# Kernel tuning notes

Measured on AMD Instinct MI355X. Metric: run time of the kernel, lower is better.

Reference implementation:

```python
import jax, jax.numpy as jnp
import numpy as np

DIM = 1024
HDIM = 128
SEQ = 2048
B = 4
NHEADS = DIM // HDIM


def _decay_mask(seq_len, gamma):
    idx = jnp.arange(seq_len, dtype=jnp.float32)
    # gamma ** (i - j), lower-triangular (i >= j), else 0
    D = gamma ** (idx[:, None] - idx[None, :])
    D = jnp.where(idx[:, None] >= idx[None, :], D, 0.0)
    return D.astype(jnp.float32)


def setup_inputs() -> dict:
    key = jax.random.key(0)
    ks = jax.random.split(key, 8)
    q = jax.random.normal(ks[0], (B, SEQ, DIM), dtype=jnp.float32)
    k = jax.random.normal(ks[1], (B, SEQ, DIM), dtype=jnp.float32)
    v = jax.random.normal(ks[2], (B, SEQ, DIM), dtype=jnp.float32)
    # per-head shared QKV weight (source reuses one Dense for Q,K,V)
    scale = 1.0 / np.sqrt(HDIM)
    W_qkv = jax.random.normal(ks[3], (NHEADS, HDIM, HDIM), dtype=jnp.float32) * scale
    # gate: Dense(dim, bias, swish); output: Dense(dim, bias)
    Wg = jax.random.normal(ks[4], (DIM, DIM), dtype=jnp.float32) / np.sqrt(DIM)
    bg = jnp.zeros((DIM,), dtype=jnp.float32)
    Wo = jax.random.normal(ks[5], (DIM, DIM), dtype=jnp.float32) / np.sqrt(DIM)
    bo = jnp.zeros((DIM,), dtype=jnp.float32)
    # GroupNormalization(scale=False): default groups=32, center=True -> beta only
    beta = jnp.zeros((DIM,), dtype=jnp.float32)
    return {"q": q, "k": k, "v": v, "W_qkv": W_qkv, "Wg": Wg, "bg": bg,
            "Wo": Wo, "bo": bo, "beta": beta}


def _retention_head(qh, kh, vh, W, D):
    # qh,kh,vh: [B,S,HDIM]; source bug: all three come from q, and the
    # single shared Dense W projects each.
    Q = qh @ W
    K = kh @ W
    V = vh @ W
    x = jnp.einsum('bsd,btd->bst', Q, K) / jnp.sqrt(jnp.float32(HDIM))
    # D normalized: D / sqrt(sum over axis 1 (rows), broadcast over rows)
    Dn = D / jnp.sqrt(jnp.sum(D, axis=0))  # tf.reduce_sum(D,1) on [S,S]: axis=1 of 2D = cols? see note
    x = x * Dn
    # row-norm: divide by max(|sum over axis 1 of each [S,S] slice|, 1)
    s = jnp.sum(x, axis=1, keepdims=True)  # per-sample, tf axis 1 of [S,S]
    x = x / jnp.maximum(jnp.abs(s), 1.0)
    return jnp.einsum('bst,btd->bsd', x, V)


def _group_norm(x, beta, groups=32, eps=1e-3):
    b, s, c = x.shape
    xg = x.reshape(b, s, groups, c // groups)
    mu = jnp.mean(xg, axis=-1, keepdims=True)
    var = jnp.var(xg, axis=-1, keepdims=True)
    xn = (xg - mu) / jnp.sqrt(var + eps)
    return xn.reshape(b, s, c) + beta


def reference(q, k, v, W_qkv, Wg, bg, Wo, bo, beta):
    gammas = 1.0 - 2.0 ** (-5.0 - jnp.arange(NHEADS, dtype=jnp.float32))
    Wgate = jax.nn.swish(q @ Wg + bg)
    # source bug: splits q for Q, K, V alike
    qs = q.reshape(B, SEQ, NHEADS, HDIM)
    outs = []
    idx = jnp.arange(SEQ, dtype=jnp.float32)
    lower = idx[:, None] >= idx[None, :]
    for h in range(NHEADS):
        D = jnp.where(lower, gammas[h] ** (idx[:, None] - idx[None, :]), 0.0)
        qh = qs[:, :, h, :]
        outs.append(_retention_head(qh, qh, qh, W_qkv[h], D))
    x = jnp.concatenate(outs, axis=-1)
    Y = _group_norm(x, beta)
    return (Wgate * Y) @ Wo + bo
```

## Files before the change

kernel.cpp:

```cpp
#include <hip/hip_runtime.h>


constexpr int SEQ  = 2048;
constexpr int BATCH= 4;
constexpr int DIM  = 1024;
constexpr int HDIM = 128;
constexpr int NH   = 8;
constexpr int NBH  = BATCH * NH;
constexpr int NC   = 16;
constexpr int CCH  = 32;
constexpr int NCC  = SEQ / CCH;

typedef __bf16 bf16x8 __attribute__((ext_vector_type(8)));
typedef float  f32x4  __attribute__((ext_vector_type(4)));

__device__ __forceinline__ f32x4 mfma16(bf16x8 a, bf16x8 b, f32x4 c) {
  return __builtin_amdgcn_mfma_f32_16x16x32_bf16(a, b, c, 0, 0, 0);
}

__device__ __forceinline__ float bf2f(unsigned short u) {
  return __builtin_bit_cast(float, (unsigned int)u << 16);
}
__device__ __forceinline__ unsigned short f2bf(float f) {
  unsigned int x = __builtin_bit_cast(unsigned int, f);
  x += 0x7fffu + ((x >> 16) & 1u);
  return (unsigned short)(x >> 16);
}

__device__ __forceinline__ int swz(int row, int col, int RS) {
  int cb  = col >> 3;
  int scb = (cb & ~7) | ((cb ^ (row >> 1)) & 7);
  return row * RS + scb * 8 + (col & 7);
}

__device__ __forceinline__ uint4 pack8(float4 a, float4 b) {
  uint4 o;
  o.x = (unsigned int)f2bf(a.x) | ((unsigned int)f2bf(a.y) << 16);
  o.y = (unsigned int)f2bf(a.z) | ((unsigned int)f2bf(a.w) << 16);
  o.z = (unsigned int)f2bf(b.x) | ((unsigned int)f2bf(b.y) << 16);
  o.w = (unsigned int)f2bf(b.z) | ((unsigned int)f2bf(b.w) << 16);
  return o;
}

__global__ void detect(const unsigned short* __restrict__ q, int* __restrict__ flag)
{
  int lane = threadIdx.x;
  int sane = 0;
  for (int i = lane; i < 1024; i += 64) {
    int e = (q[i] >> 7) & 0xFF;
    sane += (e >= 100 && e <= 140) ? 1 : 0;
  }
  #pragma unroll
  for (int o = 1; o < 64; o <<= 1) sane += __shfl_xor(sane, o);
  if (lane == 0) flag[0] = (sane >= 900) ? 1 : 0;
}

__global__ __launch_bounds__(256) void wtrans(const void* __restrict__ src,
    unsigned short* __restrict__ dst, int rows, int cols,
    const int* __restrict__ dflag)
{
  __shared__ float tile[64][65];
  const int isbf = dflag[0];
  const size_t moff = (size_t)blockIdx.z * rows * cols;
  const int r0 = blockIdx.y * 64, c0 = blockIdx.x * 64;
  const int tr = threadIdx.x >> 4;
  const int tc = (threadIdx.x & 15) * 4;

  #pragma unroll
  for (int rr = 0; rr < 64; rr += 16) {
    int r = r0 + rr + tr;
    if (isbf) {
      const unsigned short* s = (const unsigned short*)src + moff + (size_t)r * cols + c0 + tc;
      tile[rr + tr][tc + 0] = bf2f(s[0]);
      tile[rr + tr][tc + 1] = bf2f(s[1]);
      tile[rr + tr][tc + 2] = bf2f(s[2]);
      tile[rr + tr][tc + 3] = bf2f(s[3]);
    } else {
      float4 v = *(const float4*)((const float*)src + moff + (size_t)r * cols + c0 + tc);
      tile[rr + tr][tc + 0] = v.x;
      tile[rr + tr][tc + 1] = v.y;
      tile[rr + tr][tc + 2] = v.z;
      tile[rr + tr][tc + 3] = v.w;
    }
  }
  __syncthreads();

  const int n  = threadIdx.x >> 2;
  const int kg = (threadIdx.x & 3) * 16;
  unsigned int ov[8];
  #pragma unroll
  for (int j = 0; j < 8; ++j) {
    unsigned short lo = f2bf(tile[kg + 2 * j + 0][n]);
    unsigned short hi = f2bf(tile[kg + 2 * j + 1][n]);
    ov[j] = (unsigned int)lo | ((unsigned int)hi << 16);
  }
  unsigned short* d = dst + moff + (size_t)(c0 + n) * rows + r0 + kg;
  ((uint4*)d)[0] = make_uint4(ov[0], ov[1], ov[2], ov[3]);
  ((uint4*)d)[1] = make_uint4(ov[4], ov[5], ov[6], ov[7]);
}

__global__ __launch_bounds__(256, 4) void gemm128(
    const void* __restrict__ A, int lda,
    const unsigned short* __restrict__ B, int ldb, int K,
    const void* __restrict__ bias, int act,
    void* __restrict__ out, int mode, int adt, int obf,
    const int* __restrict__ dflag)
{
  __shared__ __align__(16) unsigned short As[128 * 64];
  __shared__ __align__(16) unsigned short Bs[128 * 64];
  const int isbf = dflag[0];
  const int abf  = (adt == 1) || (adt == 2 && isbf);
  const int tid  = threadIdx.x;
  const int lane = tid & 63;
  const int w    = tid >> 6;
  const int wy   = w >> 1, wx = w & 1;
  const int m15  = lane & 15, qd = lane >> 4;

  int bx = blockIdx.x, by = blockIdx.y;
  if (mode == 0) {
    int nwg = gridDim.x * gridDim.y;
    int lin = by * gridDim.x + bx;
    int qq = nwg >> 3, rr = nwg & 7;
    int xcd = lin & 7, idx = lin >> 3;
    int wg = (xcd < rr) ? xcd * (qq + 1) + idx
                        : rr * (qq + 1) + (xcd - rr) * qq + idx;
    bx = wg % gridDim.x;
    by = wg / gridDim.x;
  }

  const size_t aoff = (mode == 1) ? (size_t)blockIdx.z * 128 : 0;
  const size_t boff = (mode == 1) ? (size_t)blockIdx.z * 128 * 128 : 0;
  const size_t arow = (size_t)(by * 128);
  const size_t bcol = (size_t)(bx * 128);

  f32x4 zero4 = {0.0f, 0.0f, 0.0f, 0.0f};
  f32x4 acc[4][4];
  #pragma unroll
  for (int i = 0; i < 4; ++i)
    #pragma unroll
    for (int j = 0; j < 4; ++j) acc[i][j] = zero4;

  const int kIters = K >> 6;
  for (int kt = 0; kt < kIters; ++kt) {
    __syncthreads();
    if (abf) {
      const unsigned short* pa = (const unsigned short*)A + aoff + arow * lda + kt * 64;
      #pragma unroll
      for (int g = 0; g < 4; ++g) {
        int idx = tid + g * 256;
        int r = idx >> 3, cb = idx & 7;
        *(uint4*)&As[swz(r, cb * 8, 64)] = *(const uint4*)(pa + (size_t)r * lda + cb * 8);
      }
    } else {
      const float* pa = (const float*)A + aoff + arow * lda + kt * 64;
      #pragma unroll
      for (int g = 0; g < 4; ++g) {
        int idx = tid + g * 256;
        int r = idx >> 3, cb = idx & 7;
        float4 f0 = *(const float4*)(pa + (size_t)r * lda + cb * 8);
        float4 f1 = *(const float4*)(pa + (size_t)r * lda + cb * 8 + 4);
        *(uint4*)&As[swz(r, cb * 8, 64)] = pack8(f0, f1);
      }
    }
    {
      const unsigned short* pb = B + boff + bcol * (size_t)ldb + kt * 64;
      #pragma unroll
      for (int g = 0; g < 4; ++g) {
        int idx = tid + g * 256;
        int r = idx >> 3, cb = idx & 7;
        *(uint4*)&Bs[swz(r, cb * 8, 64)] = *(const uint4*)(pb + (size_t)r * ldb + cb * 8);
      }
    }
    __syncthreads();
    #pragma unroll
    for (int kk = 0; kk < 2; ++kk) {
      bf16x8 af[4], bfr[4];
      #pragma unroll
      for (int mt = 0; mt < 4; ++mt)
        af[mt] = *(const bf16x8*)&As[swz(wy * 64 + mt * 16 + m15, kk * 32 + qd * 8, 64)];
      #pragma unroll
      for (int nt = 0; nt < 4; ++nt)
        bfr[nt] = *(const bf16x8*)&Bs[swz(wx * 64 + nt * 16 + m15, kk * 32 + qd * 8, 64)];
      #pragma unroll
      for (int mt = 0; mt < 4; ++mt)
        #pragma unroll
        for (int nt = 0; nt < 4; ++nt)
          acc[mt][nt] = mfma16(af[mt], bfr[nt], acc[mt][nt]);
    }
  }

  const int obf_eff = (obf == 2) ? (isbf ? 1 : 0) : obf;
  #pragma unroll
  for (int mt = 0; mt < 4; ++mt)
    #pragma unroll
    for (int nt = 0; nt < 4; ++nt) {
      int nl = wx * 64 + nt * 16 + m15;
      int n  = bx * 128 + nl;
      float bv = 0.0f;
      if (bias) bv = isbf ? bf2f(((const unsigned short*)bias)[n]) : ((const float*)bias)[n];
      #pragma unroll
      for (int r = 0; r < 4; ++r) {
        int ml = wy * 64 + mt * 16 + qd * 4 + r;
        int m  = by * 128 + ml;
        float v = acc[mt][nt][r] + bv;
        if (act == 1) v = v / (1.0f + __expf(-v));
        if (mode == 0) {
          size_t oi = (size_t)m * (gridDim.x * 128) + n;
          if (obf_eff) ((unsigned short*)out)[oi] = f2bf(v);
          else         ((float*)out)[oi] = v;
        } else {
          int b = m >> 11, s = m & 2047;
          size_t bh = (size_t)(b * NH + blockIdx.z);
          ((unsigned short*)out)[(bh * SEQ + s) * HDIM + n] = f2bf(v);
        }
      }
    }
}

__global__ __launch_bounds__(128) void kzcA(const unsigned short* __restrict__ X,
                                            float* __restrict__ L)
{
  const int d  = threadIdx.x;
  const int cc = blockIdx.x;
  const int bh = blockIdx.y;
  const int h  = bh & 7;
  const float gam = 1.0f - exp2f(-5.0f - (float)h);
  const unsigned short* Xb = X + (size_t)bh * SEQ * HDIM + (size_t)cc * CCH * HDIM;
  float z = 0.0f;
  #pragma unroll
  for (int i = CCH - 1; i >= 0; --i)
    z = bf2f(Xb[(size_t)i * HDIM + d]) + gam * z;
  L[((size_t)bh * NCC + cc) * HDIM + d] = z;
}

__global__ __launch_bounds__(128) void kzcB(float* __restrict__ L)
{
  const int d  = threadIdx.x;
  const int bh = blockIdx.x;
  const int h  = bh & 7;
  const float gam = 1.0f - exp2f(-5.0f - (float)h);
  const float g32 = exp2f(log2f(gam) * (float)CCH);
  float z = 0.0f;
  for (int cc = NCC - 1; cc >= 0; --cc) {
    size_t i = ((size_t)bh * NCC + cc) * HDIM + d;
    float lc = L[i];
    L[i] = z;
    z = lc + g32 * z;
  }
}

__global__ __launch_bounds__(64) void kdot2(const unsigned short* __restrict__ X,
    const float* __restrict__ Carry, float* __restrict__ U)
{
  const int lane = threadIdx.x;
  const int cc   = blockIdx.x;
  const int bh   = blockIdx.y;
  const int h    = bh & 7;
  const float gam    = 1.0f - exp2f(-5.0f - (float)h);
  const float l2g    = log2f(gam);
  const float inv1mg = exp2f(5.0f + (float)h);
  const float c1     = 0.08838834764831845f;
  const unsigned short* Xb = X + (size_t)bh * SEQ * HDIM + (size_t)cc * CCH * HDIM;
  float2 cr = *(const float2*)(Carry + ((size_t)bh * NCC + cc) * HDIM + lane * 2);
  float z0 = 0.0f, z1 = 0.0f;
  float coeff = gam;
  float keep = 0.0f;
  #pragma unroll
  for (int i = 0; i < CCH; ++i) {
    const int t = CCH - 1 - i;
    unsigned int xu = *(const unsigned int*)(Xb + (size_t)t * HDIM + lane * 2);
    float x0 = bf2f((unsigned short)(xu & 0xffffu));
    float x1 = bf2f((unsigned short)(xu >> 16));
    z0 = x0 + gam * z0;
    z1 = x1 + gam * z1;
    float dot = x0 * (z0 + coeff * cr.x) + x1 * (z1 + coeff * cr.y);
    #pragma unroll
    for (int o = 1; o < 64; o <<= 1) dot += __shfl_xor(dot, o);
    if (lane == t) keep = dot;
    coeff *= gam;
  }
  if (lane < CCH) {
    int tg = cc * CCH + lane;
    float colD   = (1.0f - exp2f(l2g * (float)(SEQ - tg))) * inv1mg;
    float sq     = sqrtf(colD);
    float colsum = keep * c1 / sq;
    float den    = fmaxf(fabsf(colsum), 1.0f);
    U[(size_t)bh * SEQ + tg] = c1 / (sq * den);
  }
}

__global__ __launch_bounds__(256, 2) void chunkstate(
    const unsigned short* __restrict__ X,
    const float* __restrict__ U,
    unsigned short* __restrict__ G)
{
  __shared__ __align__(16) unsigned short XT [16384];
  __shared__ __align__(16) unsigned short XTs[16384];
  const int tid  = threadIdx.x;
  const int lane = tid & 63;
  const int w    = tid >> 6;
  const int wy   = w >> 1, wx = w & 1;
  const int m15  = lane & 15, qd = lane >> 4;
  const int c    = blockIdx.x;
  const int bh   = blockIdx.y;
  const int h    = bh & 7;
  const float gam = 1.0f - exp2f(-5.0f - (float)h);
  const float l2g = log2f(gam);
  const int t0 = c * 128;
  const unsigned short* Xb = X + (size_t)bh * SEQ * HDIM;
  const float* Ub = U + (size_t)bh * SEQ;

  #pragma unroll
  for (int g = 0; g < 8; ++g) {
    int idx = tid + g * 256;
    int t = idx >> 4, d0 = (idx & 15) * 8;
    uint4 w4 = *(const uint4*)(Xb + (size_t)(t0 + t) * HDIM + d0);
    float wt = exp2f(l2g * (float)(127 - t)) * Ub[t0 + t];
    const unsigned short* wp = (const unsigned short*)&w4;
    #pragma unroll
    for (int j = 0; j < 8; ++j) {
      unsigned short v = wp[j];
      XT [swz(d0 + j, t, 128)] = v;
      XTs[swz(d0 + j, t, 128)] = f2bf(bf2f(v) * wt);
    }
  }
  __syncthreads();

  f32x4 zero4 = {0.0f, 0.0f, 0.0f, 0.0f};
  f32x4 acc[4][4];
  #pragma unroll
  for (int i = 0; i < 4; ++i)
    #pragma unroll
    for (int j = 0; j < 4; ++j) acc[i][j] = zero4;

  #pragma unroll
  for (int kk = 0; kk < 4; ++kk) {
    bf16x8 af[4], bfr[4];
    #pragma unroll
    for (int mt = 0; mt < 4; ++mt)
      af[mt] = *(const bf16x8*)&XTs[swz(wy * 64 + mt * 16 + m15, kk * 32 + qd * 8, 128)];
    #pragma unroll
    for (int nt = 0; nt < 4; ++nt)
      bfr[nt] = *(const bf16x8*)&XT[swz(wx * 64 + nt * 16 + m15, kk * 32 + qd * 8, 128)];
    #pragma unroll
    for (int mt = 0; mt < 4; ++mt)
      #pragma unroll
      for (int nt = 0; nt < 4; ++nt)
        acc[mt][nt] = mfma16(af[mt], bfr[nt], acc[mt][nt]);
  }

  unsigned short* Gp = G + (((size_t)bh * NC + c) << 14);
  #pragma unroll
  for (int mt = 0; mt < 4; ++mt)
    #pragma unroll
    for (int nt = 0; nt < 4; ++nt)
      #pragma unroll
      for (int r = 0; r < 4; ++r) {
        int d1 = wy * 64 + mt * 16 + qd * 4 + r;
        int d2 = wx * 64 + nt * 16 + m15;
        Gp[(size_t)d1 * 128 + d2] = f2bf(acc[mt][nt][r]);
      }
}

__global__ __launch_bounds__(256) void scanS(unsigned short* __restrict__ GS)
{
  int gid = blockIdx.x * 256 + threadIdx.x;
  int bh = gid >> 11;
  int e8 = (gid & 2047) << 3;
  int h  = bh & 7;
  float gam  = 1.0f - exp2f(-5.0f - (float)h);
  float g128 = exp2f(log2f(gam) * 128.0f);
  float s[8];
  #pragma unroll
  for (int j = 0; j < 8; ++j) s[j] = 0.0f;
  unsigned short* base = GS + ((size_t)bh << 18) + e8;
  #pragma unroll
  for (int c = 0; c < NC; ++c) {
    uint4 v = *(uint4*)(base + ((size_t)c << 14));
    const unsigned short* wp = (const unsigned short*)&v;
    #pragma unroll
    for (int j = 0; j < 8; ++j) s[j] = g128 * s[j] + bf2f(wp[j]);
    uint4 o;
    unsigned int* op = (unsigned int*)&o;
    op[0] = (unsigned int)f2bf(s[0]) | ((unsigned int)f2bf(s[1]) << 16);
    op[1] = (unsigned int)f2bf(s[2]) | ((unsigned int)f2bf(s[3]) << 16);
    op[2] = (unsigned int)f2bf(s[4]) | ((unsigned int)f2bf(s[5]) << 16);
    op[3] = (unsigned int)f2bf(s[6]) | ((unsigned int)f2bf(s[7]) << 16);
    *(uint4*)(base + ((size_t)c << 14)) = o;
  }
}

__global__ __launch_bounds__(256, 2) void retention2(
    const unsigned short* __restrict__ X,
    const float* __restrict__ U,
    const unsigned short* __restrict__ S,
    unsigned short* __restrict__ R)
{
  __shared__ __align__(16) unsigned short Qs[16384];
  __shared__ __align__(16) unsigned short SB[16384];

  const int tid  = threadIdx.x;
  const int lane = tid & 63;
  const int w    = tid >> 6;
  const int wy   = w >> 1, wx = w & 1;
  const int m15  = lane & 15, qd = lane >> 4;
  const int c    = blockIdx.x;
  const int bh   = blockIdx.y;
  const int h    = bh & 7;
  const int b    = bh >> 3;
  const float gam = 1.0f - exp2f(-5.0f - (float)h);
  const float l2g = log2f(gam);
  const int sbase = c * 128;
  const unsigned short* Xb = X + (size_t)bh * SEQ * HDIM;
  const float* Ub = U + (size_t)bh * SEQ;

  #pragma unroll
  for (int g = 0; g < 8; ++g) {
    int idx = tid + g * 256;
    int r = idx >> 4, cb = idx & 15;
    *(uint4*)&Qs[swz(r, cb * 8, 128)] =
        *(const uint4*)(Xb + (size_t)(sbase + r) * HDIM + cb * 8);
  }
  if (c > 0) {
    const unsigned short* Sp = S + (((size_t)bh * NC + (c - 1)) << 14);
    #pragma unroll
    for (int g = 0; g < 8; ++g) {
      int idx = tid + g * 256;
      int r = idx >> 4, cb = idx & 15;
      *(uint4*)&SB[swz(r, cb * 8, 128)] = *(const uint4*)(Sp + (size_t)r * 128 + cb * 8);
    }
  }
  __syncthreads();

  bf16x8 aq[4][4];
  #pragma unroll
  for (int mt = 0; mt < 4; ++mt)
    #pragma unroll
    for (int kk = 0; kk < 4; ++kk)
      aq[mt][kk] = *(const bf16x8*)&Qs[swz(wy * 64 + mt * 16 + m15, kk * 32 + qd * 8, 128)];

  float crowL[16];
  #pragma unroll
  for (int mt = 0; mt < 4; ++mt)
    #pragma unroll
    for (int r = 0; r < 4; ++r)
      crowL[mt * 4 + r] = exp2f(l2g * (float)(wy * 64 + mt * 16 + qd * 4 + r));

  f32x4 zero4 = {0.0f, 0.0f, 0.0f, 0.0f};
  f32x4 oacc[4][4];
  #pragma unroll
  for (int i = 0; i < 4; ++i)
    #pragma unroll
    for (int j = 0; j < 4; ++j) oacc[i][j] = zero4;

  if (c > 0) {
    #pragma unroll
    for (int kk = 0; kk < 4; ++kk) {
      bf16x8 bs[4];
      #pragma unroll
      for (int nt = 0; nt < 4; ++nt)
        bs[nt] = *(const bf16x8*)&SB[swz(wx * 64 + nt * 16 + m15, kk * 32 + qd * 8, 128)];
      #pragma unroll
      for (int mt = 0; mt < 4; ++mt)
        #pragma unroll
        for (int nt = 0; nt < 4; ++nt)
          oacc[mt][nt] = mfma16(aq[mt][kk], bs[nt], oacc[mt][nt]);
    }
    #pragma unroll
    for (int mt = 0; mt < 4; ++mt) {
      #pragma unroll
      for (int r = 0; r < 4; ++r) {
        float f = crowL[mt * 4 + r] * gam;
        #pragma unroll
        for (int nt = 0; nt < 4; ++nt) oacc[mt][nt][r] *= f;
      }
    }
  }

  unsigned short* VsT = SB;
  unsigned short* Ps  = SB + 8192;

  for (int th = 0; th < 2; ++th) {
    const int t0 = th * 64;
    f32x4 pacc[4][2];
    #pragma unroll
    for (int i = 0; i < 4; ++i) { pacc[i][0] = zero4; pacc[i][1] = zero4; }
    #pragma unroll
    for (int kk = 0; kk < 4; ++kk) {
      bf16x8 bk[2];
      #pragma unroll
      for (int nt = 0; nt < 2; ++nt)
        bk[nt] = *(const bf16x8*)&Qs[swz(t0 + wx * 32 + nt * 16 + m15, kk * 32 + qd * 8, 128)];
      #pragma unroll
      for (int mt = 0; mt < 4; ++mt)
        #pragma unroll
        for (int nt = 0; nt < 2; ++nt)
          pacc[mt][nt] = mfma16(aq[mt][kk], bk[nt], pacc[mt][nt]);
    }
    __syncthreads();

    #pragma unroll
    for (int g = 0; g < 4; ++g) {
      int idx = tid + g * 256;
      int t = idx & 63, d0 = (idx >> 6) * 8;
      uint4 w4 = *(const uint4*)(Xb + (size_t)(sbase + t0 + t) * HDIM + d0);
      const unsigned short* wp = (const unsigned short*)&w4;
      #pragma unroll
      for (int j = 0; j < 8; ++j)
        VsT[swz(d0 + j, t, 64)] = wp[j];
    }
    #pragma unroll
    for (int nt = 0; nt < 2; ++nt) {
      int tloc = t0 + wx * 32 + nt * 16 + m15;
      float cf = exp2f(-l2g * (float)tloc) * Ub[sbase + tloc];
      #pragma unroll
      for (int mt = 0; mt < 4; ++mt)
        #pragma unroll
        for (int r = 0; r < 4; ++r) {
          int sl = wy * 64 + mt * 16 + qd * 4 + r;
          float v = (sl >= tloc) ? pacc[mt][nt][r] * crowL[mt * 4 + r] * cf : 0.0f;
          Ps[swz(sl, tloc - t0, 64)] = f2bf(v);
        }
    }
    __syncthreads();
    #pragma unroll
    for (int kk = 0; kk < 2; ++kk) {
      bf16x8 ap[4], bv[4];
      #pragma unroll
      for (int mt = 0; mt < 4; ++mt)
        ap[mt] = *(const bf16x8*)&Ps[swz(wy * 64 + mt * 16 + m15, kk * 32 + qd * 8, 64)];
      #pragma unroll
      for (int nt = 0; nt < 4; ++nt)
        bv[nt] = *(const bf16x8*)&VsT[swz(wx * 64 + nt * 16 + m15, kk * 32 + qd * 8, 64)];
      #pragma unroll
      for (int mt = 0; mt < 4; ++mt)
        #pragma unroll
        for (int nt = 0; nt < 4; ++nt)
          oacc[mt][nt] = mfma16(ap[mt], bv[nt], oacc[mt][nt]);
    }
  }

  #pragma unroll
  for (int mt = 0; mt < 4; ++mt)
    #pragma unroll
    for (int nt = 0; nt < 4; ++nt)
      #pragma unroll
      for (int r = 0; r < 4; ++r) {
        int sg = sbase + wy * 64 + mt * 16 + qd * 4 + r;
        int n  = wx * 64 + nt * 16 + m15;
        R[(size_t)(b * SEQ + sg) * DIM + h * HDIM + n] = f2bf(oacc[mt][nt][r]);
      }
}

__global__ __launch_bounds__(256) void gn_gate(const unsigned short* __restrict__ R,
    const void* __restrict__ beta, unsigned short* __restrict__ GU,
    const int* __restrict__ dflag)
{
  const int isbf = dflag[0];
  const int row = blockIdx.x;
  const int t   = threadIdx.x;
  uint2 xv = *(const uint2*)(R + (size_t)row * DIM + t * 4);
  float x0 = bf2f((unsigned short)(xv.x & 0xffffu)), x1 = bf2f((unsigned short)(xv.x >> 16));
  float x2 = bf2f((unsigned short)(xv.y & 0xffffu)), x3 = bf2f((unsigned short)(xv.y >> 16));
  float s  = x0 + x1 + x2 + x3;
  float ss = x0 * x0 + x1 * x1 + x2 * x2 + x3 * x3;
  #pragma unroll
  for (int m = 1; m <= 4; m <<= 1) {
    s  += __shfl_xor(s, m, 8);
    ss += __shfl_xor(ss, m, 8);
  }
  float mean = s * (1.0f / 32.0f);
  float var  = ss * (1.0f / 32.0f) - mean * mean;
  float rstd = rsqrtf(var + 1e-3f);
  float b0, b1, b2, b3;
  if (isbf) {
    uint2 bv = *(const uint2*)((const unsigned short*)beta + t * 4);
    b0 = bf2f((unsigned short)(bv.x & 0xffffu)); b1 = bf2f((unsigned short)(bv.x >> 16));
    b2 = bf2f((unsigned short)(bv.y & 0xffffu)); b3 = bf2f((unsigned short)(bv.y >> 16));
  } else {
    float4 bv = *(const float4*)((const float*)beta + t * 4);
    b0 = bv.x; b1 = bv.y; b2 = bv.z; b3 = bv.w;
  }
  uint2 gv = *(const uint2*)(GU + (size_t)row * DIM + t * 4);
  float g0 = bf2f((unsigned short)(gv.x & 0xffffu)), g1 = bf2f((unsigned short)(gv.x >> 16));
  float g2 = bf2f((unsigned short)(gv.y & 0xffffu)), g3 = bf2f((unsigned short)(gv.y >> 16));
  unsigned short u0 = f2bf(((x0 - mean) * rstd + b0) * g0);
  unsigned short u1 = f2bf(((x1 - mean) * rstd + b1) * g1);
  unsigned short u2 = f2bf(((x2 - mean) * rstd + b2) * g2);
  unsigned short u3 = f2bf(((x3 - mean) * rstd + b3) * g3);
  uint2 o;
  o.x = (unsigned int)u0 | ((unsigned int)u1 << 16);
  o.y = (unsigned int)u2 | ((unsigned int)u3 << 16);
  *(uint2*)(GU + (size_t)row * DIM + t * 4) = o;
}

extern "C" void kernel_launch(void* const* d_in, const int* in_sizes, int n_in,
                              void* d_out, int out_size, void* d_ws, size_t ws_size,
                              hipStream_t stream)
{
  (void)in_sizes; (void)n_in; (void)out_size; (void)ws_size;
  const void* q    = d_in[0];
  const void* Wqkv = d_in[3];
  const void* Wg   = d_in[4];
  const void* bg   = d_in[5];
  const void* Wo   = d_in[6];
  const void* bo   = d_in[7];
  const void* beta = d_in[8];

  char* p = (char*)d_ws;
  auto take = [&](size_t bytes) { char* r = p; p += (bytes + 255) & ~(size_t)255; return r; };
  int*  flag = (int*)take(256);
  unsigned short* X  = (unsigned short*)take((size_t)NBH * SEQ * HDIM * 2);
  float* U     = (float*)take((size_t)NBH * SEQ * 4);
  unsigned short* WqkvT = (unsigned short*)take((size_t)NH * HDIM * HDIM * 2);
  unsigned short* WgT   = (unsigned short*)take((size_t)DIM * DIM * 2);
  unsigned short* WoT   = (unsigned short*)take((size_t)DIM * DIM * 2);
  unsigned short* Rb = (unsigned short*)d_out;
  unsigned short* GS = (unsigned short*)((char*)d_out + (size_t)16 * 1024 * 1024);
  float* Carry = (float*)GS;
  unsigned short* Gg = X;

  detect<<<1, 64, 0, stream>>>((const unsigned short*)q, flag);

  wtrans<<<dim3(16, 16, 1), 256, 0, stream>>>(Wg,   WgT,   DIM,  DIM,  flag);
  wtrans<<<dim3(16, 16, 1), 256, 0, stream>>>(Wo,   WoT,   DIM,  DIM,  flag);
  wtrans<<<dim3(2, 2, NH),  256, 0, stream>>>(Wqkv, WqkvT, HDIM, HDIM, flag);

  gemm128<<<dim3(1, 64, NH), 256, 0, stream>>>(q, DIM, WqkvT, HDIM, HDIM,
                                               nullptr, 0, X, 1, 2, 1, flag);

  kzcA <<<dim3(NCC, NBH), 128, 0, stream>>>(X, Carry);
  kzcB <<<NBH, 128, 0, stream>>>(Carry);
  kdot2<<<dim3(NCC, NBH), 64, 0, stream>>>(X, Carry, U);

  chunkstate<<<dim3(NC, NBH), 256, 0, stream>>>(X, U, GS);
  scanS     <<<256, 256, 0, stream>>>(GS);
  retention2<<<dim3(NC, NBH), 256, 0, stream>>>(X, U, GS, Rb);

  gemm128<<<dim3(8, 64, 1), 256, 0, stream>>>(q, DIM, WgT, DIM, DIM, bg, 1,
                                              Gg, 0, 2, 1, flag);

  gn_gate<<<dim3(BATCH * SEQ, 1, 1), 256, 0, stream>>>(Rb, beta, Gg, flag);

  gemm128<<<dim3(8, 64, 1), 256, 0, stream>>>(Gg, DIM, WoT, DIM, DIM, bo, 0,
                                              d_out, 0, 1, 2, flag);
}
```

Before: 345.8 us.

## Pre-convert q to bf16, use direct global-to-LDS loads, coalesce epilogue stores

Adds a kernel that converts q to bf16 once into workspace so both the QKV and gate GEMMs take the bf16 path. The GEMM tile loads use global_load_lds to write directly into swizzled LDS instead of going through registers. The epilogues of the head-projection GEMM, chunkstate and retention2 stage results through LDS so global stores are 16-byte coalesced rather than scattered 2-byte writes. The cost is an extra conversion pass over q plus more workspace and extra barriers in the epilogues.

```diff
diff --git a/kernel.cpp b/kernel.cpp
--- a/kernel.cpp
+++ b/kernel.cpp
@@ -33,6 +33,12 @@
   return row * RS + scb * 8 + (col & 7);
 }
 
+typedef const __attribute__((address_space(1))) unsigned int* gas_t;
+typedef __attribute__((address_space(3))) unsigned int* las_t;
+__device__ __forceinline__ void gl_lds16(const unsigned short* g, unsigned short* l) {
+  __builtin_amdgcn_global_load_lds((gas_t)g, (las_t)l, 16, 0, 0);
+}
+
 __device__ __forceinline__ uint4 pack8(float4 a, float4 b) {
   uint4 o;
   o.x = (unsigned int)f2bf(a.x) | ((unsigned int)f2bf(a.y) << 16);
@@ -53,6 +59,19 @@
   #pragma unroll
   for (int o = 1; o < 64; o <<= 1) sane += __shfl_xor(sane, o);
   if (lane == 0) flag[0] = (sane >= 900) ? 1 : 0;
+}
+
+__global__ __launch_bounds__(256) void qbf(const void* __restrict__ q,
+    unsigned short* __restrict__ qb, const int* __restrict__ dflag)
+{
+  const int idx = blockIdx.x * 256 + threadIdx.x;
+  if (dflag[0]) {
+    ((uint4*)qb)[idx] = ((const uint4*)q)[idx];
+  } else {
+    float4 a = ((const float4*)q)[2 * idx];
+    float4 b = ((const float4*)q)[2 * idx + 1];
+    ((uint4*)qb)[idx] = pack8(a, b);
+  }
 }
 
 __global__ __launch_bounds__(256) void wtrans(const void* __restrict__ src,
@@ -115,6 +134,9 @@
   const int w    = tid >> 6;
   const int wy   = w >> 1, wx = w & 1;
   const int m15  = lane & 15, qd = lane >> 4;
+  const int w8  = w * 8;
+  const int lr  = lane >> 3;
+  const int scb = lane & 7;
 
   int bx = blockIdx.x, by = blockIdx.y;
   if (mode == 0) {
@@ -147,9 +169,9 @@
       const unsigned short* pa = (const unsigned short*)A + aoff + arow * lda + kt * 64;
       #pragma unroll
       for (int g = 0; g < 4; ++g) {
-        int idx = tid + g * 256;
-        int r = idx >> 3, cb = idx & 7;
-        *(uint4*)&As[swz(r, cb * 8, 64)] = *(const uint4*)(pa + (size_t)r * lda + cb * 8);
+        int r  = g * 32 + w8 + lr;
+        int cb = scb ^ ((r >> 1) & 7);
+        gl_lds16(pa + (size_t)r * lda + cb * 8, &As[g * 2048 + w * 512]);
       }
     } else {
       const float* pa = (const float*)A + aoff + arow * lda + kt * 64;
@@ -166,9 +188,9 @@
       const unsigned short* pb = B + boff + bcol * (size_t)ldb + kt * 64;
       #pragma unroll
       for (int g = 0; g < 4; ++g) {
-        int idx = tid + g * 256;
-        int r = idx >> 3, cb = idx & 7;
-        *(uint4*)&Bs[swz(r, cb * 8, 64)] = *(const uint4*)(pb + (size_t)r * ldb + cb * 8);
+        int r  = g * 32 + w8 + lr;
+        int cb = scb ^ ((r >> 1) & 7);
+        gl_lds16(pb + (size_t)r * ldb + cb * 8, &Bs[g * 2048 + w * 512]);
       }
     }
     __syncthreads();
@@ -190,6 +212,38 @@
   }
 
   const int obf_eff = (obf == 2) ? (isbf ? 1 : 0) : obf;
+  if (mode == 1) {
+    #pragma unroll
+    for (int half = 0; half < 2; ++half) {
+      __syncthreads();
+      if (wy == half) {
+        #pragma unroll
+        for (int mt = 0; mt < 4; ++mt)
+          #pragma unroll
+          for (int nt = 0; nt < 4; ++nt) {
+            int n = wx * 64 + nt * 16 + m15;
+            #pragma unroll
+            for (int r = 0; r < 4; ++r) {
+              int sl = mt * 16 + qd * 4 + r;
+              As[swz(sl, n, 128)] = f2bf(acc[mt][nt][r]);
+            }
+          }
+      }
+      __syncthreads();
+      #pragma unroll
+      for (int g = 0; g < 4; ++g) {
+        int idx = tid + g * 256;
+        int rr = idx >> 4, cbb = idx & 15;
+        int m = by * 128 + half * 64 + rr;
+        int b = m >> 11, s = m & 2047;
+        size_t bh = (size_t)(b * NH + blockIdx.z);
+        *(uint4*)&((unsigned short*)out)[(bh * SEQ + s) * HDIM + cbb * 8] =
+            *(const uint4*)&As[swz(rr, cbb * 8, 128)];
+      }
+    }
+    return;
+  }
+
   #pragma unroll
   for (int mt = 0; mt < 4; ++mt)
     #pragma unroll
@@ -204,15 +258,9 @@
         int m  = by * 128 + ml;
         float v = acc[mt][nt][r] + bv;
         if (act == 1) v = v / (1.0f + __expf(-v));
-        if (mode == 0) {
-          size_t oi = (size_t)m * (gridDim.x * 128) + n;
-          if (obf_eff) ((unsigned short*)out)[oi] = f2bf(v);
-          else         ((float*)out)[oi] = v;
-        } else {
-          int b = m >> 11, s = m & 2047;
-          size_t bh = (size_t)(b * NH + blockIdx.z);
-          ((unsigned short*)out)[(bh * SEQ + s) * HDIM + n] = f2bf(v);
-        }
+        size_t oi = (size_t)m * (gridDim.x * 128) + n;
+        if (obf_eff) ((unsigned short*)out)[oi] = f2bf(v);
+        else         ((float*)out)[oi] = v;
       }
     }
 }
@@ -351,15 +399,30 @@
 
   unsigned short* Gp = G + (((size_t)bh * NC + c) << 14);
   #pragma unroll
-  for (int mt = 0; mt < 4; ++mt)
-    #pragma unroll
-    for (int nt = 0; nt < 4; ++nt)
-      #pragma unroll
-      for (int r = 0; r < 4; ++r) {
-        int d1 = wy * 64 + mt * 16 + qd * 4 + r;
-        int d2 = wx * 64 + nt * 16 + m15;
-        Gp[(size_t)d1 * 128 + d2] = f2bf(acc[mt][nt][r]);
-      }
+  for (int half = 0; half < 2; ++half) {
+    __syncthreads();
+    if (wy == half) {
+      #pragma unroll
+      for (int mt = 0; mt < 4; ++mt)
+        #pragma unroll
+        for (int nt = 0; nt < 4; ++nt) {
+          int d2 = wx * 64 + nt * 16 + m15;
+          #pragma unroll
+          for (int r = 0; r < 4; ++r) {
+            int dl = mt * 16 + qd * 4 + r;
+            XT[swz(dl, d2, 128)] = f2bf(acc[mt][nt][r]);
+          }
+        }
+    }
+    __syncthreads();
+    #pragma unroll
+    for (int g = 0; g < 4; ++g) {
+      int idx = tid + g * 256;
+      int rr = idx >> 4, cbb = idx & 15;
+      *(uint4*)&Gp[(size_t)(half * 64 + rr) * 128 + cbb * 8] =
+          *(const uint4*)&XT[swz(rr, cbb * 8, 128)];
+    }
+  }
 }
 
 __global__ __launch_bounds__(256) void scanS(unsigned short* __restrict__ GS)
@@ -540,16 +603,26 @@
     }
   }
 
+  __syncthreads();
   #pragma unroll
   for (int mt = 0; mt < 4; ++mt)
     #pragma unroll
-    for (int nt = 0; nt < 4; ++nt)
+    for (int nt = 0; nt < 4; ++nt) {
+      int n = wx * 64 + nt * 16 + m15;
       #pragma unroll
       for (int r = 0; r < 4; ++r) {
-        int sg = sbase + wy * 64 + mt * 16 + qd * 4 + r;
-        int n  = wx * 64 + nt * 16 + m15;
-        R[(size_t)(b * SEQ + sg) * DIM + h * HDIM + n] = f2bf(oacc[mt][nt][r]);
+        int sl = wy * 64 + mt * 16 + qd * 4 + r;
+        SB[swz(sl, n, 128)] = f2bf(oacc[mt][nt][r]);
       }
+    }
+  __syncthreads();
+  #pragma unroll
+  for (int g = 0; g < 8; ++g) {
+    int idx = tid + g * 256;
+    int rr = idx >> 4, cbb = idx & 15;
+    *(uint4*)&R[(size_t)(b * SEQ + sbase + rr) * DIM + h * HDIM + cbb * 8] =
+        *(const uint4*)&SB[swz(rr, cbb * 8, 128)];
+  }
 }
 
 __global__ __launch_bounds__(256) void gn_gate(const unsigned short* __restrict__ R,
@@ -598,7 +671,7 @@
                               void* d_out, int out_size, void* d_ws, size_t ws_size,
                               hipStream_t stream)
 {
-  (void)in_sizes; (void)n_in; (void)out_size; (void)ws_size;
+  (void)in_sizes; (void)n_in; (void)out_size;
   const void* q    = d_in[0];
   const void* Wqkv = d_in[3];
   const void* Wg   = d_in[4];
@@ -615,6 +688,9 @@
   unsigned short* WqkvT = (unsigned short*)take((size_t)NH * HDIM * HDIM * 2);
   unsigned short* WgT   = (unsigned short*)take((size_t)DIM * DIM * 2);
   unsigned short* WoT   = (unsigned short*)take((size_t)DIM * DIM * 2);
+  size_t qbBytes = (size_t)BATCH * SEQ * DIM * 2;
+  unsigned short* qb = (unsigned short*)take(qbBytes);
+  const bool useQb = ((size_t)(p - (char*)d_ws) <= ws_size);
   unsigned short* Rb = (unsigned short*)d_out;
   unsigned short* GS = (unsigned short*)((char*)d_out + (size_t)16 * 1024 * 1024);
   float* Carry = (float*)GS;
@@ -625,9 +701,14 @@
   wtrans<<<dim3(16, 16, 1), 256, 0, stream>>>(Wg,   WgT,   DIM,  DIM,  flag);
   wtrans<<<dim3(16, 16, 1), 256, 0, stream>>>(Wo,   WoT,   DIM,  DIM,  flag);
   wtrans<<<dim3(2, 2, NH),  256, 0, stream>>>(Wqkv, WqkvT, HDIM, HDIM, flag);
-
-  gemm128<<<dim3(1, 64, NH), 256, 0, stream>>>(q, DIM, WqkvT, HDIM, HDIM,
-                                               nullptr, 0, X, 1, 2, 1, flag);
+  if (useQb)
+    qbf<<<4096, 256, 0, stream>>>(q, qb, flag);
+
+  const void* Aq = useQb ? (const void*)qb : q;
+  const int   adtq = useQb ? 1 : 2;
+
+  gemm128<<<dim3(1, 64, NH), 256, 0, stream>>>(Aq, DIM, WqkvT, HDIM, HDIM,
+                                               nullptr, 0, X, 1, adtq, 1, flag);
 
   kzcA <<<dim3(NCC, NBH), 128, 0, stream>>>(X, Carry);
   kzcB <<<NBH, 128, 0, stream>>>(Carry);
@@ -637,8 +718,8 @@
   scanS     <<<256, 256, 0, stream>>>(GS);
   retention2<<<dim3(NC, NBH), 256, 0, stream>>>(X, U, GS, Rb);
 
-  gemm128<<<dim3(8, 64, 1), 256, 0, stream>>>(q, DIM, WgT, DIM, DIM, bg, 1,
-                                              Gg, 0, 2, 1, flag);
+  gemm128<<<dim3(8, 64, 1), 256, 0, stream>>>(Aq, DIM, WgT, DIM, DIM, bg, 1,
+                                              Gg, 0, adtq, 1, flag);
 
   gn_gate<<<dim3(BATCH * SEQ, 1, 1), 256, 0, stream>>>(Rb, beta, Gg, flag);
 
```

Measured after the change: 321.5 us. -7.0%, faster.
